# Kernel tuning notes

Measured on AMD Instinct MI355X. Metric: run time of the kernel, lower is better.

The kernel has to match this reference:

```python
import jax, jax.numpy as jnp
import numpy as np


def setup_inputs() -> dict:
    key = jax.random.key(0)
    uvs = jax.random.normal(key, (16, 16, 512, 256), dtype=jnp.float32)
    return {"uvs": uvs}


def reference(uvs):
    # uvs: [B, 2K, m, d] -> u, v: [B, K, m, d]
    u, v = jnp.split(uvs, 2, axis=1)
    # Row-sum of (u @ v^T) over n equals u @ sum_n(v); same math, avoids [B,K,m,m] intermediate.
    left_gate = jax.nn.relu(jnp.sign(jnp.einsum('bkmd,bkd->bkm', u, v.sum(axis=2))))[..., None]
    # Col-sum of (u @ v^T) over m equals v @ sum_m(u).
    right_gate = jax.nn.relu(jnp.sign(jnp.einsum('bknd,bkd->bkn', v, u.sum(axis=2))))[..., None]
    return jnp.concatenate([left_gate * u, right_gate * v], axis=1)
```

## Files before the change

### kernel.cpp

```cpp
#include <hip/hip_runtime.h>
#include <hip/hip_bf16.h>


#define B_ 16
#define J_ 16
#define M_ 512
#define D_ 256
#define D4_ 64
#define S_ 4

typedef float f32x4 __attribute__((ext_vector_type(4)));

__global__ __launch_bounds__(256) void k_colsum(const float4* __restrict__ in,
                                                float4* __restrict__ part) {
    const int blk = blockIdx.x;
    const int s  = blk & (S_ - 1);
    const int bj = blk >> 2;
    const int t  = threadIdx.x;
    const int l  = t & 63;
    const int w  = t >> 6;

    const float4* base = in + (size_t)bj * (M_ * D4_) + (size_t)(s * 128 + w) * D4_ + l;

    float4 acc = make_float4(0.f, 0.f, 0.f, 0.f);
#pragma unroll 8
    for (int i = 0; i < 32; ++i) {
        float4 v = base[(size_t)(4 * i) * D4_];
        acc.x += v.x; acc.y += v.y; acc.z += v.z; acc.w += v.w;
    }

    __shared__ float4 red[256];
    red[t] = acc;
    __syncthreads();
    if (t < 64) {
        float4 a = red[t], b = red[t + 64], c = red[t + 128], d = red[t + 192];
        float4 r;
        r.x = (a.x + b.x) + (c.x + d.x);
        r.y = (a.y + b.y) + (c.y + d.y);
        r.z = (a.z + b.z) + (c.z + d.z);
        r.w = (a.w + b.w) + (c.w + d.w);
        part[(size_t)(bj * S_ + s) * D4_ + t] = r;
    }
}

__global__ __launch_bounds__(256) void k_gate(const float4* __restrict__ in,
                                              const float4* __restrict__ part,
                                              float4* __restrict__ out) {
    const int blk   = blockIdx.x;
    const int chunk = blk & 7;
    const int bj    = blk >> 3;
    const int b     = bj >> 4;
    const int j     = bj & 15;
    const int jp    = (j < 8) ? (j + 8) : (j - 8);
    const int t     = threadIdx.x;
    const int l     = t & 63;
    const int w     = t >> 6;

    const int pbase = (b * J_ + jp) * (S_ * D4_) + l;
    float4 s0 = part[pbase], s1 = part[pbase + 64],
           s2 = part[pbase + 128], s3 = part[pbase + 192];
    float4 sv;
    sv.x = (s0.x + s1.x) + (s2.x + s3.x);
    sv.y = (s0.y + s1.y) + (s2.y + s3.y);
    sv.z = (s0.z + s1.z) + (s2.z + s3.z);
    sv.w = (s0.w + s1.w) + (s2.w + s3.w);

    const size_t rowbase = (size_t)bj * (M_ * D4_) + (size_t)(chunk * 64 + w * 16) * D4_ + l;
    const float4* inb = in + rowbase;
    f32x4* outb = (f32x4*)(out + rowbase);

#pragma unroll 4
    for (int r = 0; r < 16; ++r) {
        float4 v = inb[(size_t)r * D4_];
        float p = v.x * sv.x + v.y * sv.y + v.z * sv.z + v.w * sv.w;
#pragma unroll
        for (int off = 32; off; off >>= 1) p += __shfl_xor(p, off, 64);
        float g = (p > 0.f) ? 1.f : 0.f;
        f32x4 o;
        o.x = v.x * g; o.y = v.y * g; o.z = v.z * g; o.w = v.w * g;
        __builtin_nontemporal_store(o, outb + (size_t)r * D4_);
    }
}

extern "C" void kernel_launch(void* const* d_in, const int* in_sizes, int n_in,
                              void* d_out, int out_size, void* d_ws, size_t ws_size,
                              hipStream_t stream) {
    const float4* in  = (const float4*)d_in[0];
    float4*       out = (float4*)d_out;
    float4*       part = (float4*)d_ws;

    k_colsum<<<B_ * J_ * S_, 256, 0, stream>>>(in, part);
    k_gate<<<B_ * J_ * (M_ / 64), 256, 0, stream>>>(in, part, out);
}
```

Baseline: 65.75 us.

## Fuse u column-sum into u gating pass to cut one full read

```diff
diff --git a/kernel.cpp b/kernel.cpp
--- a/kernel.cpp
+++ b/kernel.cpp
@@ -2,30 +2,31 @@
 #include <hip/hip_bf16.h>
 
 
-#define B_ 16
-#define J_ 16
-#define M_ 512
-#define D_ 256
+#define B_  16
+#define J_  16
+#define K_  8
+#define M_  512
 #define D4_ 64
-#define S_ 4
+#define S_  8
 
 typedef float f32x4 __attribute__((ext_vector_type(4)));
 
-__global__ __launch_bounds__(256) void k_colsum(const float4* __restrict__ in,
-                                                float4* __restrict__ part) {
+__global__ __launch_bounds__(256) void k_vsum(const float4* __restrict__ in,
+                                              float4* __restrict__ vpart) {
     const int blk = blockIdx.x;
-    const int s  = blk & (S_ - 1);
-    const int bj = blk >> 2;
-    const int t  = threadIdx.x;
-    const int l  = t & 63;
-    const int w  = t >> 6;
+    const int s   = blk & (S_ - 1);
+    const int bk  = blk >> 3;
+    const int b   = bk >> 3, k = bk & 7;
+    const int t   = threadIdx.x;
+    const int l   = t & 63;
+    const int w   = t >> 6;
 
-    const float4* base = in + (size_t)bj * (M_ * D4_) + (size_t)(s * 128 + w) * D4_ + l;
+    const float4* base = in + ((size_t)(b * J_ + 8 + k) * M_ + s * 64 + w * 16) * D4_ + l;
 
     float4 acc = make_float4(0.f, 0.f, 0.f, 0.f);
-#pragma unroll 8
-    for (int i = 0; i < 32; ++i) {
-        float4 v = base[(size_t)(4 * i) * D4_];
+#pragma unroll
+    for (int i = 0; i < 16; ++i) {
+        float4 v = base[(size_t)i * D4_];
         acc.x += v.x; acc.y += v.y; acc.z += v.z; acc.w += v.w;
     }
 
@@ -33,51 +34,96 @@
     red[t] = acc;
     __syncthreads();
     if (t < 64) {
-        float4 a = red[t], b = red[t + 64], c = red[t + 128], d = red[t + 192];
+        float4 a = red[t], c = red[t + 64], d = red[t + 128], e = red[t + 192];
         float4 r;
-        r.x = (a.x + b.x) + (c.x + d.x);
-        r.y = (a.y + b.y) + (c.y + d.y);
-        r.z = (a.z + b.z) + (c.z + d.z);
-        r.w = (a.w + b.w) + (c.w + d.w);
-        part[(size_t)(bj * S_ + s) * D4_ + t] = r;
+        r.x = (a.x + c.x) + (d.x + e.x);
+        r.y = (a.y + c.y) + (d.y + e.y);
+        r.z = (a.z + c.z) + (d.z + e.z);
+        r.w = (a.w + c.w) + (d.w + e.w);
+        vpart[(size_t)(bk * S_ + s) * 64 + t] = r;
     }
 }
 
-__global__ __launch_bounds__(256) void k_gate(const float4* __restrict__ in,
-                                              const float4* __restrict__ part,
-                                              float4* __restrict__ out) {
-    const int blk   = blockIdx.x;
-    const int chunk = blk & 7;
-    const int bj    = blk >> 3;
-    const int b     = bj >> 4;
-    const int j     = bj & 15;
-    const int jp    = (j < 8) ? (j + 8) : (j - 8);
-    const int t     = threadIdx.x;
-    const int l     = t & 63;
-    const int w     = t >> 6;
+__global__ __launch_bounds__(256) void k_upass(const float4* __restrict__ in,
+                                               const float4* __restrict__ vpart,
+                                               float4* __restrict__ upart,
+                                               float4* __restrict__ out) {
+    const int blk = blockIdx.x;
+    const int s   = blk & (S_ - 1);
+    const int bk  = blk >> 3;
+    const int b   = bk >> 3, k = bk & 7;
+    const int t   = threadIdx.x;
+    const int l   = t & 63;
+    const int w   = t >> 6;
 
-    const int pbase = (b * J_ + jp) * (S_ * D4_) + l;
-    float4 s0 = part[pbase], s1 = part[pbase + 64],
-           s2 = part[pbase + 128], s3 = part[pbase + 192];
-    float4 sv;
-    sv.x = (s0.x + s1.x) + (s2.x + s3.x);
-    sv.y = (s0.y + s1.y) + (s2.y + s3.y);
-    sv.z = (s0.z + s1.z) + (s2.z + s3.z);
-    sv.w = (s0.w + s1.w) + (s2.w + s3.w);
+    float4 sv = make_float4(0.f, 0.f, 0.f, 0.f);
+#pragma unroll
+    for (int q = 0; q < S_; ++q) {
+        float4 p = vpart[(size_t)(bk * S_ + q) * 64 + l];
+        sv.x += p.x; sv.y += p.y; sv.z += p.z; sv.w += p.w;
+    }
 
-    const size_t rowbase = (size_t)bj * (M_ * D4_) + (size_t)(chunk * 64 + w * 16) * D4_ + l;
-    const float4* inb = in + rowbase;
-    f32x4* outb = (f32x4*)(out + rowbase);
+    const size_t rowbase = ((size_t)(b * J_ + k) * M_ + s * 64 + w * 16) * D4_ + l;
+    const f32x4* inb  = (const f32x4*)(in + rowbase);
+    f32x4*       outb = (f32x4*)(out + rowbase);
+
+    float4 acc = make_float4(0.f, 0.f, 0.f, 0.f);
+#pragma unroll 4
+    for (int r = 0; r < 16; ++r) {
+        f32x4 v = __builtin_nontemporal_load(inb + (size_t)r * D4_);
+        acc.x += v.x; acc.y += v.y; acc.z += v.z; acc.w += v.w;
+        float p = v.x * sv.x + v.y * sv.y + v.z * sv.z + v.w * sv.w;
+#pragma unroll
+        for (int off = 32; off; off >>= 1) p += __shfl_xor(p, off, 64);
+        float g = (p > 0.f) ? 1.f : 0.f;
+        f32x4 o; o.x = v.x * g; o.y = v.y * g; o.z = v.z * g; o.w = v.w * g;
+        __builtin_nontemporal_store(o, outb + (size_t)r * D4_);
+    }
+
+    __shared__ float4 red[256];
+    red[t] = acc;
+    __syncthreads();
+    if (t < 64) {
+        float4 a = red[t], c = red[t + 64], d = red[t + 128], e = red[t + 192];
+        float4 r;
+        r.x = (a.x + c.x) + (d.x + e.x);
+        r.y = (a.y + c.y) + (d.y + e.y);
+        r.z = (a.z + c.z) + (d.z + e.z);
+        r.w = (a.w + c.w) + (d.w + e.w);
+        upart[(size_t)(bk * S_ + s) * 64 + t] = r;
+    }
+}
+
+__global__ __launch_bounds__(256) void k_vpass(const float4* __restrict__ in,
+                                               const float4* __restrict__ upart,
+                                               float4* __restrict__ out) {
+    const int blk = blockIdx.x;
+    const int s   = blk & (S_ - 1);
+    const int bk  = blk >> 3;
+    const int b   = bk >> 3, k = bk & 7;
+    const int t   = threadIdx.x;
+    const int l   = t & 63;
+    const int w   = t >> 6;
+
+    float4 su = make_float4(0.f, 0.f, 0.f, 0.f);
+#pragma unroll
+    for (int q = 0; q < S_; ++q) {
+        float4 p = upart[(size_t)(bk * S_ + q) * 64 + l];
+        su.x += p.x; su.y += p.y; su.z += p.z; su.w += p.w;
+    }
+
+    const size_t rowbase = ((size_t)(b * J_ + 8 + k) * M_ + s * 64 + w * 16) * D4_ + l;
+    const float4* inb  = in + rowbase;
+    f32x4*        outb = (f32x4*)(out + rowbase);
 
 #pragma unroll 4
     for (int r = 0; r < 16; ++r) {
         float4 v = inb[(size_t)r * D4_];
-        float p = v.x * sv.x + v.y * sv.y + v.z * sv.z + v.w * sv.w;
+        float p = v.x * su.x + v.y * su.y + v.z * su.z + v.w * su.w;
 #pragma unroll
         for (int off = 32; off; off >>= 1) p += __shfl_xor(p, off, 64);
         float g = (p > 0.f) ? 1.f : 0.f;
-        f32x4 o;
-        o.x = v.x * g; o.y = v.y * g; o.z = v.z * g; o.w = v.w * g;
+        f32x4 o; o.x = v.x * g; o.y = v.y * g; o.z = v.z * g; o.w = v.w * g;
         __builtin_nontemporal_store(o, outb + (size_t)r * D4_);
     }
 }
@@ -87,8 +133,11 @@
                               hipStream_t stream) {
     const float4* in  = (const float4*)d_in[0];
     float4*       out = (float4*)d_out;
-    float4*       part = (float4*)d_ws;
+    float4* vpart = (float4*)d_ws;
+    float4* upart = (float4*)((char*)d_ws + (1u << 20));
 
-    k_colsum<<<B_ * J_ * S_, 256, 0, stream>>>(in, part);
-    k_gate<<<B_ * J_ * (M_ / 64), 256, 0, stream>>>(in, part, out);
+    const int grid = B_ * K_ * S_;
+    k_vsum <<<grid, 256, 0, stream>>>(in, vpart);
+    k_upass<<<grid, 256, 0, stream>>>(in, vpart, upart, out);
+    k_vpass<<<grid, 256, 0, stream>>>(in, upart, out);
 }
```

Result: faster. 64.13 us (-2.5%).

## Fuse colsum and gate into one cooperative kernel keeping v in registers

Applied to the files above, without the earlier changes.

```diff
diff --git a/kernel.cpp b/kernel.cpp
--- a/kernel.cpp
+++ b/kernel.cpp
@@ -1,94 +1,97 @@
 #include <hip/hip_runtime.h>
-#include <hip/hip_bf16.h>
+#include <hip/hip_cooperative_groups.h>
+
+namespace cg = cooperative_groups;
 
 
-#define B_ 16
-#define J_ 16
-#define M_ 512
-#define D_ 256
-#define D4_ 64
-#define S_ 4
+#define NBLK 256
+#define NTHR 1024
 
 typedef float f32x4 __attribute__((ext_vector_type(4)));
 
-__global__ __launch_bounds__(256) void k_colsum(const float4* __restrict__ in,
-                                                float4* __restrict__ part) {
+__global__ __launch_bounds__(NTHR, 4) void k_fused(const f32x4* __restrict__ in,
+                                                   f32x4* __restrict__ out,
+                                                   f32x4* __restrict__ vpart,
+                                                   f32x4* __restrict__ upart) {
+    cg::grid_group grid = cg::this_grid();
     const int blk = blockIdx.x;
-    const int s  = blk & (S_ - 1);
-    const int bj = blk >> 2;
-    const int t  = threadIdx.x;
-    const int l  = t & 63;
-    const int w  = t >> 6;
+    const int s   = blk & 1;
+    const int bk  = blk >> 1;
+    const int b   = bk >> 3, k = bk & 7;
+    const int t   = threadIdx.x;
+    const int l   = t & 63;
+    const int w   = t >> 6;
 
-    const float4* base = in + (size_t)bj * (M_ * D4_) + (size_t)(s * 128 + w) * D4_ + l;
+    const size_t vbase = ((size_t)((b * 16 + 8 + k) * 512) + s * 256 + w * 16) * 64 + l;
+    const size_t ubase = ((size_t)((b * 16 + k) * 512) + s * 256 + w * 16) * 64 + l;
 
-    float4 acc = make_float4(0.f, 0.f, 0.f, 0.f);
-#pragma unroll 8
-    for (int i = 0; i < 32; ++i) {
-        float4 v = base[(size_t)(4 * i) * D4_];
-        acc.x += v.x; acc.y += v.y; acc.z += v.z; acc.w += v.w;
+    __shared__ f32x4 red[NTHR];
+
+    f32x4 vreg[16];
+    f32x4 acc = {0.f, 0.f, 0.f, 0.f};
+#pragma unroll
+    for (int i = 0; i < 16; ++i) {
+        vreg[i] = __builtin_nontemporal_load(in + vbase + (size_t)i * 64);
+        acc += vreg[i];
     }
-
-    __shared__ float4 red[256];
     red[t] = acc;
     __syncthreads();
     if (t < 64) {
-        float4 a = red[t], b = red[t + 64], c = red[t + 128], d = red[t + 192];
-        float4 r;
-        r.x = (a.x + b.x) + (c.x + d.x);
-        r.y = (a.y + b.y) + (c.y + d.y);
-        r.z = (a.z + b.z) + (c.z + d.z);
-        r.w = (a.w + b.w) + (c.w + d.w);
-        part[(size_t)(bj * S_ + s) * D4_ + t] = r;
+        f32x4 r = {0.f, 0.f, 0.f, 0.f};
+#pragma unroll
+        for (int q = 0; q < 16; ++q) r += red[q * 64 + t];
+        vpart[(size_t)blk * 64 + t] = r;
     }
-}
 
-__global__ __launch_bounds__(256) void k_gate(const float4* __restrict__ in,
-                                              const float4* __restrict__ part,
-                                              float4* __restrict__ out) {
-    const int blk   = blockIdx.x;
-    const int chunk = blk & 7;
-    const int bj    = blk >> 3;
-    const int b     = bj >> 4;
-    const int j     = bj & 15;
-    const int jp    = (j < 8) ? (j + 8) : (j - 8);
-    const int t     = threadIdx.x;
-    const int l     = t & 63;
-    const int w     = t >> 6;
+    grid.sync();
 
-    const int pbase = (b * J_ + jp) * (S_ * D4_) + l;
-    float4 s0 = part[pbase], s1 = part[pbase + 64],
-           s2 = part[pbase + 128], s3 = part[pbase + 192];
-    float4 sv;
-    sv.x = (s0.x + s1.x) + (s2.x + s3.x);
-    sv.y = (s0.y + s1.y) + (s2.y + s3.y);
-    sv.z = (s0.z + s1.z) + (s2.z + s3.z);
-    sv.w = (s0.w + s1.w) + (s2.w + s3.w);
-
-    const size_t rowbase = (size_t)bj * (M_ * D4_) + (size_t)(chunk * 64 + w * 16) * D4_ + l;
-    const float4* inb = in + rowbase;
-    f32x4* outb = (f32x4*)(out + rowbase);
-
+    const f32x4 vs = vpart[(size_t)(bk * 2 + 0) * 64 + l] +
+                     vpart[(size_t)(bk * 2 + 1) * 64 + l];
+    f32x4 uacc = {0.f, 0.f, 0.f, 0.f};
 #pragma unroll 4
-    for (int r = 0; r < 16; ++r) {
-        float4 v = inb[(size_t)r * D4_];
-        float p = v.x * sv.x + v.y * sv.y + v.z * sv.z + v.w * sv.w;
+    for (int i = 0; i < 16; ++i) {
+        f32x4 uv = __builtin_nontemporal_load(in + ubase + (size_t)i * 64);
+        uacc += uv;
+        float p = uv.x * vs.x + uv.y * vs.y + uv.z * vs.z + uv.w * vs.w;
 #pragma unroll
         for (int off = 32; off; off >>= 1) p += __shfl_xor(p, off, 64);
-        float g = (p > 0.f) ? 1.f : 0.f;
-        f32x4 o;
-        o.x = v.x * g; o.y = v.y * g; o.z = v.z * g; o.w = v.w * g;
-        __builtin_nontemporal_store(o, outb + (size_t)r * D4_);
+        const float g = (p > 0.f) ? 1.f : 0.f;
+        __builtin_nontemporal_store(uv * g, out + ubase + (size_t)i * 64);
+    }
+    __syncthreads();
+    red[t] = uacc;
+    __syncthreads();
+    if (t < 64) {
+        f32x4 r = {0.f, 0.f, 0.f, 0.f};
+#pragma unroll
+        for (int q = 0; q < 16; ++q) r += red[q * 64 + t];
+        upart[(size_t)blk * 64 + t] = r;
+    }
+
+    grid.sync();
+
+    const f32x4 us = upart[(size_t)(bk * 2 + 0) * 64 + l] +
+                     upart[(size_t)(bk * 2 + 1) * 64 + l];
+#pragma unroll
+    for (int i = 0; i < 16; ++i) {
+        float p = vreg[i].x * us.x + vreg[i].y * us.y +
+                  vreg[i].z * us.z + vreg[i].w * us.w;
+#pragma unroll
+        for (int off = 32; off; off >>= 1) p += __shfl_xor(p, off, 64);
+        const float g = (p > 0.f) ? 1.f : 0.f;
+        __builtin_nontemporal_store(vreg[i] * g, out + vbase + (size_t)i * 64);
     }
 }
 
 extern "C" void kernel_launch(void* const* d_in, const int* in_sizes, int n_in,
                               void* d_out, int out_size, void* d_ws, size_t ws_size,
                               hipStream_t stream) {
-    const float4* in  = (const float4*)d_in[0];
-    float4*       out = (float4*)d_out;
-    float4*       part = (float4*)d_ws;
+    const f32x4* in  = (const f32x4*)d_in[0];
+    f32x4*       out = (f32x4*)d_out;
+    f32x4* vpart = (f32x4*)d_ws;
+    f32x4* upart = (f32x4*)((char*)d_ws + (256u << 10));
 
-    k_colsum<<<B_ * J_ * S_, 256, 0, stream>>>(in, part);
-    k_gate<<<B_ * J_ * (M_ / 64), 256, 0, stream>>>(in, part, out);
+    void* args[] = { (void*)&in, (void*)&out, (void*)&vpart, (void*)&upart };
+    hipLaunchCooperativeKernel((void*)k_fused, dim3(NBLK), dim3(NTHR),
+                               args, 0, stream);
 }
```

After: 116.5 us. 1.77x slower.
